# Kernel tuning notes

Hardware: AMD Instinct MI355X
Metric: run time of the kernel (lower is better)

Reference implementation:

```python
import jax, jax.numpy as jnp
import numpy as np

D_MODEL = 1024
NUM_EXPERTS = 8


def setup_inputs() -> dict:
    key = jax.random.key(0)
    k_x, k_wg, k_bg, k_we, k_be = jax.random.split(key, 5)
    B, S, D, E = 4, 2048, D_MODEL, NUM_EXPERTS
    x = jax.random.normal(k_x, (B, S, D), dtype=jnp.float32)
    # gate: nn.Linear(d_model, num_experts) -> weight [E, D], bias [E]
    Wg = jax.random.normal(k_wg, (E, D), dtype=jnp.float32) * 0.02
    bg = jax.random.normal(k_bg, (E,), dtype=jnp.float32) * 0.02
    # experts: E x nn.Linear(d_model, d_model) -> weights [E, D, D], biases [E, D]
    We = jax.random.normal(k_we, (E, D, D), dtype=jnp.float32) * 0.02
    be = jax.random.normal(k_be, (E, D), dtype=jnp.float32) * 0.02
    return {"x": x, "Wg": Wg, "bg": bg, "We": We, "be": be, "top_k": 2}


def reference(x, Wg, bg, We, be, top_k):
    # gate_scores: softmax over experts. x:[B,S,D], Wg:[E,D] -> [B,S,E]
    gate_scores = jax.nn.softmax(jnp.einsum("bsd,ed->bse", x, Wg) + bg, axis=-1)
    top_k_values, top_k_indices = jax.lax.top_k(gate_scores, top_k)  # [B,S,K]
    # dense all-expert compute (faithful to original): [B,S,D,E]
    expert_outputs = jnp.einsum("bsd,ekd->bske", x, We) + be.T  # be.T: [D,E]
    # gather top-k experts along last dim: idx broadcast over feature dim D
    top_k_outputs = jnp.take_along_axis(
        expert_outputs, top_k_indices[:, :, None, :], axis=-1
    )  # [B,S,D,K]
    weighted = (top_k_outputs * top_k_values[:, :, None, :]).sum(axis=-1)  # [B,S,D]
    return weighted
```

## Files before the change

### kernel.cpp

```cpp
#include <hip/hip_runtime.h>
#include <hip/hip_bf16.h>
#include <stdint.h>

#define D_MODEL 1024
#define NUM_EXPERTS 8
#define NBUCKET 16
#define BM 128
#define BN 128
#define BK 64
#define KSTEPS (D_MODEL / BK)
#define GATE_TOK 32
#define GATE_BLOCKS 256
#define CONV_BLOCKS 2048
#define NSEG (NUM_EXPERTS * KSTEPS * 1024 * 8)

typedef __bf16 bf16x8 __attribute__((ext_vector_type(8)));
typedef float f32x4 __attribute__((ext_vector_type(4)));
typedef unsigned short u16x8 __attribute__((ext_vector_type(8)));

__device__ __forceinline__ unsigned short f32_to_bf16_rne(float f) {
    union { float f; uint32_t u; } v;
    v.f = f;
    uint32_t u = v.u;
    u += 0x7FFFu + ((u >> 16) & 1u);
    return (unsigned short)(u >> 16);
}

__device__ __forceinline__ float bf16_to_f32(unsigned short h) {
    union { uint32_t u; float f; } v;
    v.u = ((uint32_t)h) << 16;
    return v.f;
}

__device__ __forceinline__ void gload_lds16(const unsigned short* g, unsigned short* l) {
    __builtin_amdgcn_global_load_lds(
        (const __attribute__((address_space(1))) void*)g,
        (__attribute__((address_space(3))) void*)l,
        16, 0, 0);
}

__global__ __launch_bounds__(512) void prep_kernel(
    const float* __restrict__ x, const float* __restrict__ Wg,
    const float* __restrict__ bg, const float* __restrict__ We, int T,
    int* __restrict__ counts, int* __restrict__ token_list,
    float* __restrict__ gate_list, unsigned short* __restrict__ xb,
    unsigned short* __restrict__ wbv)
{
    const int tid = threadIdx.x;

    if (blockIdx.x >= GATE_BLOCKS) {
        int g = (blockIdx.x - GATE_BLOCKS) * 512 + tid;
        int s   = g & 7;
        int kt  = (g >> 3) & (KSTEPS - 1);
        int n   = (g >> 7) & 1023;
        int e   = g >> 17;

        const float* sp = We + (size_t)g * 8;
        float4 a = ((const float4*)sp)[0];
        float4 b = ((const float4*)sp)[1];
        u16x8 o;
        o[0] = f32_to_bf16_rne(a.x);
        o[1] = f32_to_bf16_rne(a.y);
        o[2] = f32_to_bf16_rne(a.z);
        o[3] = f32_to_bf16_rne(a.w);
        o[4] = f32_to_bf16_rne(b.x);
        o[5] = f32_to_bf16_rne(b.y);
        o[6] = f32_to_bf16_rne(b.z);
        o[7] = f32_to_bf16_rne(b.w);

        int ss = s ^ (n & 7);
        unsigned short* dp =
            wbv + (((size_t)(e * KSTEPS + kt) * 1024 + n) * BK) + ss * 8;
        *(u16x8*)dp = o;
        return;
    }

    const int lane = tid & 63;
    const int wave = tid >> 6;
    const int tokBase = blockIdx.x * GATE_TOK;

    __shared__ float4 WgS[NUM_EXPERTS * 256];
    __shared__ double logitS[GATE_TOK][NUM_EXPERTS];
    __shared__ int cntS[NBUCKET];
    __shared__ int baseS[NBUCKET];

    if (tid < NBUCKET) cntS[tid] = 0;
#pragma unroll
    for (int i = 0; i < 4; i++)
        WgS[i * 512 + tid] = ((const float4*)Wg)[i * 512 + tid];
    __syncthreads();

    for (int tt = 0; tt < GATE_TOK / 8; tt++) {
        const int lt = wave * (GATE_TOK / 8) + tt;
        const int token = tokBase + lt;
        const float4* xr4 = (const float4*)(x + (size_t)token * D_MODEL);
        ushort4* xbr4 = (ushort4*)(xb + (size_t)token * D_MODEL);

        float4 xv[4];
#pragma unroll
        for (int q = 0; q < 4; q++) {
            float4 f = xr4[q * 64 + lane];
            xv[q] = f;
            ushort4 o;
            o.x = f32_to_bf16_rne(f.x);
            o.y = f32_to_bf16_rne(f.y);
            o.z = f32_to_bf16_rne(f.z);
            o.w = f32_to_bf16_rne(f.w);
            xbr4[q * 64 + lane] = o;
        }

        double acc[NUM_EXPERTS];
#pragma unroll
        for (int e = 0; e < NUM_EXPERTS; e++) {
            double a = 0.0;
#pragma unroll
            for (int q = 0; q < 4; q++) {
                float4 w = WgS[e * 256 + q * 64 + lane];
                a += (double)xv[q].x * (double)w.x;
                a += (double)xv[q].y * (double)w.y;
                a += (double)xv[q].z * (double)w.z;
                a += (double)xv[q].w * (double)w.w;
            }
            acc[e] = a;
        }
#pragma unroll
        for (int e = 0; e < NUM_EXPERTS; e++) {
            double a = acc[e];
            for (int off = 32; off > 0; off >>= 1) a += __shfl_xor(a, off, 64);
            acc[e] = a;
        }
        if (lane == 0) {
#pragma unroll
            for (int e = 0; e < NUM_EXPERTS; e++)
                logitS[lt][e] = acc[e] + (double)bg[e];
        }
    }
    __syncthreads();

    int i1 = 0, i2 = 0, o1 = 0, o2 = 0;
    double v1d = 0.0, v2d = 0.0;
    const int token2 = tokBase + tid;
    if (tid < GATE_TOK) {
        double lg[NUM_EXPERTS];
#pragma unroll
        for (int e = 0; e < NUM_EXPERTS; e++) lg[e] = logitS[tid][e];
        i1 = 0;
#pragma unroll
        for (int e = 1; e < NUM_EXPERTS; e++) if (lg[e] > lg[i1]) i1 = e;
        i2 = (i1 == 0) ? 1 : 0;
#pragma unroll
        for (int e = 0; e < NUM_EXPERTS; e++)
            if (e != i1 && lg[e] > lg[i2]) i2 = e;
        double m = lg[i1], den = 0.0;
#pragma unroll
        for (int e = 0; e < NUM_EXPERTS; e++) den += exp(lg[e] - m);
        v1d = exp(lg[i1] - m) / den;
        v2d = exp(lg[i2] - m) / den;
        o1 = atomicAdd(&cntS[i1], 1);
        o2 = atomicAdd(&cntS[8 + i2], 1);
    }
    __syncthreads();
    if (tid < NBUCKET) baseS[tid] = atomicAdd(&counts[tid], cntS[tid]);
    __syncthreads();
    if (tid < GATE_TOK) {
        int p1 = i1 * T + baseS[i1] + o1;
        token_list[p1] = token2;
        gate_list[p1]  = (float)v1d;
        int p2 = (8 + i2) * T + baseS[8 + i2] + o2;
        token_list[p2] = token2;
        gate_list[p2]  = (float)v2d;
    }
}

__global__ __launch_bounds__(512) void moe_gemm(
    const unsigned short* __restrict__ xb,
    const unsigned short* __restrict__ wb,
    const float* __restrict__ be,
    const int* __restrict__ counts,
    const int* __restrict__ token_list,
    const float* __restrict__ gate_list,
    unsigned short* __restrict__ ybuf,
    int T)
{
    const int bid = blockIdx.x;
    const int nt = bid & 7;
    const int rest = bid >> 3;
    const int vexp = rest & (NBUCKET - 1);
    const int mt = rest >> 4;
    const int e_w = vexp & 7;

    const int n_e = counts[vexp];
    const int m0 = mt * BM;
    if (m0 >= n_e) return;
    const int n0 = nt * BN;
    const int tid = threadIdx.x;

    __shared__ __align__(16) unsigned short As[2][BM * BK];
    __shared__ __align__(16) unsigned short Bs[2][BN * BK];
    __shared__ int   tokS[BM];
    __shared__ float gateS[BM];

    if (tid < BM) {
        int r = m0 + tid;
        int tk = 0; float gv = 0.f;
        if (r < n_e) {
            tk = token_list[vexp * T + r];
            gv = gate_list[vexp * T + r];
        }
        tokS[tid]  = tk;
        gateS[tid] = gv;
    }
    __syncthreads();

    const unsigned short* asrc[2];
#pragma unroll
    for (int i = 0; i < 2; i++) {
        int flat = i * 512 + tid;
        int r = flat >> 3, seg = flat & 7;
        int ss = seg ^ (r & 7);
        asrc[i] = xb + (size_t)tokS[r] * D_MODEL + ss * 8;
    }
    const unsigned short* bsrc =
        wb + (size_t)e_w * (KSTEPS * 1024 * BK) + (size_t)n0 * BK;

    const int wave = tid >> 6, lane = tid & 63;
    const int wm = (wave >> 2) * 64, wn = (wave & 3) * 32;
    const int frow = lane & 15;
    const int qq = lane >> 4;
    const int sw8 = frow & 7;

    f32x4 acc[4][2];
#pragma unroll
    for (int mi = 0; mi < 4; mi++)
#pragma unroll
        for (int ni = 0; ni < 2; ni++)
            acc[mi][ni] = (f32x4){0.f, 0.f, 0.f, 0.f};

#pragma unroll
    for (int i = 0; i < 2; i++) {
        int flat = i * 512 + tid;
        gload_lds16(asrc[i], &As[0][flat * 8]);
        gload_lds16(bsrc + flat * 8, &Bs[0][flat * 8]);
    }

#pragma unroll 2
    for (int kt = 0; kt < KSTEPS; kt++) {
        const int cur = kt & 1;
        if (kt + 1 < KSTEPS) {
#pragma unroll
            for (int i = 0; i < 2; i++) {
                int flat = i * 512 + tid;
                gload_lds16(asrc[i] + (kt + 1) * BK, &As[cur ^ 1][flat * 8]);
                gload_lds16(bsrc + (size_t)(kt + 1) * (1024 * BK) + flat * 8,
                            &Bs[cur ^ 1][flat * 8]);
            }
            asm volatile("s_waitcnt vmcnt(4)" ::: "memory");
        } else {
            asm volatile("s_waitcnt vmcnt(0)" ::: "memory");
        }
        __builtin_amdgcn_sched_barrier(0);
        __builtin_amdgcn_s_barrier();
        __builtin_amdgcn_sched_barrier(0);

#pragma unroll
        for (int ks = 0; ks < 2; ks++) {
            const int off = ((ks * 4 + qq) ^ sw8) * 8;
            bf16x8 af[4], bfv[2];
#pragma unroll
            for (int mi = 0; mi < 4; mi++)
                af[mi] = *(const bf16x8*)&As[cur][(wm + mi * 16 + frow) * BK + off];
#pragma unroll
            for (int ni = 0; ni < 2; ni++)
                bfv[ni] = *(const bf16x8*)&Bs[cur][(wn + ni * 16 + frow) * BK + off];
#pragma unroll
            for (int mi = 0; mi < 4; mi++)
#pragma unroll
                for (int ni = 0; ni < 2; ni++)
                    acc[mi][ni] = __builtin_amdgcn_mfma_f32_16x16x32_bf16(
                        af[mi], bfv[ni], acc[mi][ni], 0, 0, 0);
        }
        __builtin_amdgcn_sched_barrier(0);
        __builtin_amdgcn_s_barrier();
        __builtin_amdgcn_sched_barrier(0);
    }

    unsigned short* ybase = ybuf + (size_t)(vexp >> 3) * T * D_MODEL;
    const int rbase = (lane >> 4) * 4;
    const int col   = lane & 15;
#pragma unroll
    for (int mi = 0; mi < 4; mi++) {
#pragma unroll
        for (int r = 0; r < 4; r++) {
            int lrow = wm + mi * 16 + rbase + r;
            if (m0 + lrow < n_e) {
                int   tk = tokS[lrow];
                float gv = gateS[lrow];
                unsigned short* yr = ybase + (size_t)tk * D_MODEL;
#pragma unroll
                for (int ni = 0; ni < 2; ni++) {
                    int c = n0 + wn + ni * 16 + col;
                    float val = gv * (acc[mi][ni][r] + be[e_w * D_MODEL + c]);
                    yr[c] = f32_to_bf16_rne(val);
                }
            }
        }
    }
}

__global__ __launch_bounds__(256) void combine_kernel(
    const unsigned short* __restrict__ y0,
    const unsigned short* __restrict__ y1,
    float* __restrict__ out, int n4)
{
    int i = blockIdx.x * 256 + threadIdx.x;
    if (i >= n4) return;
    ushort4 a = ((const ushort4*)y0)[i];
    ushort4 b = ((const ushort4*)y1)[i];
    float4 o;
    o.x = bf16_to_f32(a.x) + bf16_to_f32(b.x);
    o.y = bf16_to_f32(a.y) + bf16_to_f32(b.y);
    o.z = bf16_to_f32(a.z) + bf16_to_f32(b.z);
    o.w = bf16_to_f32(a.w) + bf16_to_f32(b.w);
    ((float4*)out)[i] = o;
}

extern "C" void kernel_launch(void* const* d_in, const int* in_sizes, int n_in,
                              void* d_out, int out_size, void* d_ws, size_t ws_size,
                              hipStream_t stream) {
    const float* x  = (const float*)d_in[0];
    const float* Wg = (const float*)d_in[1];
    const float* bg = (const float*)d_in[2];
    const float* We = (const float*)d_in[3];
    const float* be = (const float*)d_in[4];

    const int T = in_sizes[0] / D_MODEL;

    char* ws = (char*)d_ws;
    unsigned short* xb = (unsigned short*)ws;
    size_t off = (size_t)T * D_MODEL * 2;
    unsigned short* wbv = (unsigned short*)(ws + off);
    off += (size_t)NUM_EXPERTS * D_MODEL * D_MODEL * 2;
    int* counts = (int*)(ws + off);         off += 256;
    int* token_list = (int*)(ws + off);     off += (size_t)NBUCKET * T * 4;
    float* gate_list = (float*)(ws + off);  off += (size_t)NBUCKET * T * 4;
    unsigned short* ybuf = (unsigned short*)(ws + off);
    off += (size_t)2 * T * D_MODEL * 2;

    hipMemsetAsync(counts, 0, 256, stream);

    prep_kernel<<<GATE_BLOCKS + CONV_BLOCKS, 512, 0, stream>>>(
        x, Wg, bg, We, T, counts, token_list, gate_list, xb, wbv);

    const int MT = (T + BM - 1) / BM;
    moe_gemm<<<MT * NBUCKET * 8, 512, 0, stream>>>(
        xb, wbv, be, counts, token_list, gate_list, ybuf, T);

    int n4c = T * D_MODEL / 4;
    combine_kernel<<<(n4c + 255) / 256, 256, 0, stream>>>(
        ybuf, ybuf + (size_t)T * D_MODEL, (float*)d_out, n4c);
}
```

Before: 231.6 us.

## Split prep kernel into separate convert and finer-grained gate kernels

Splits the fused prep kernel into a standalone weight-conversion kernel and a gate kernel. The gate kernel now uses 256-thread blocks with 8 tokens each, giving 1024 gate blocks instead of 256, so gating is spread over more CUs. Each wave handles two tokens, reading Wg directly from global memory once per pair, and the cross-lane reduction goes through shared memory plus three shuffles instead of six-step shuffles per expert. The cost is an extra kernel launch, and the gate and conversion work now run one after the other instead of sharing a single grid.

```diff
diff --git a/kernel.cpp b/kernel.cpp
--- a/kernel.cpp
+++ b/kernel.cpp
@@ -9,9 +9,7 @@
 #define BN 128
 #define BK 64
 #define KSTEPS (D_MODEL / BK)
-#define GATE_TOK 32
-#define GATE_BLOCKS 256
-#define CONV_BLOCKS 2048
+#define GATE_TOK 8
 #define NSEG (NUM_EXPERTS * KSTEPS * 1024 * 8)
 
 typedef __bf16 bf16x8 __attribute__((ext_vector_type(8)));
@@ -39,68 +37,36 @@
         16, 0, 0);
 }
 
-__global__ __launch_bounds__(512) void prep_kernel(
+__global__ __launch_bounds__(256) void gate_kernel(
     const float* __restrict__ x, const float* __restrict__ Wg,
-    const float* __restrict__ bg, const float* __restrict__ We, int T,
+    const float* __restrict__ bg, int T,
     int* __restrict__ counts, int* __restrict__ token_list,
-    float* __restrict__ gate_list, unsigned short* __restrict__ xb,
-    unsigned short* __restrict__ wbv)
+    float* __restrict__ gate_list, unsigned short* __restrict__ xb)
 {
-    const int tid = threadIdx.x;
-
-    if (blockIdx.x >= GATE_BLOCKS) {
-        int g = (blockIdx.x - GATE_BLOCKS) * 512 + tid;
-        int s   = g & 7;
-        int kt  = (g >> 3) & (KSTEPS - 1);
-        int n   = (g >> 7) & 1023;
-        int e   = g >> 17;
-
-        const float* sp = We + (size_t)g * 8;
-        float4 a = ((const float4*)sp)[0];
-        float4 b = ((const float4*)sp)[1];
-        u16x8 o;
-        o[0] = f32_to_bf16_rne(a.x);
-        o[1] = f32_to_bf16_rne(a.y);
-        o[2] = f32_to_bf16_rne(a.z);
-        o[3] = f32_to_bf16_rne(a.w);
-        o[4] = f32_to_bf16_rne(b.x);
-        o[5] = f32_to_bf16_rne(b.y);
-        o[6] = f32_to_bf16_rne(b.z);
-        o[7] = f32_to_bf16_rne(b.w);
-
-        int ss = s ^ (n & 7);
-        unsigned short* dp =
-            wbv + (((size_t)(e * KSTEPS + kt) * 1024 + n) * BK) + ss * 8;
-        *(u16x8*)dp = o;
-        return;
-    }
-
+    const int tid  = threadIdx.x;
     const int lane = tid & 63;
     const int wave = tid >> 6;
     const int tokBase = blockIdx.x * GATE_TOK;
 
-    __shared__ float4 WgS[NUM_EXPERTS * 256];
+    __shared__ double red[4][NUM_EXPERTS][65];
     __shared__ double logitS[GATE_TOK][NUM_EXPERTS];
     __shared__ int cntS[NBUCKET];
     __shared__ int baseS[NBUCKET];
 
     if (tid < NBUCKET) cntS[tid] = 0;
-#pragma unroll
-    for (int i = 0; i < 4; i++)
-        WgS[i * 512 + tid] = ((const float4*)Wg)[i * 512 + tid];
-    __syncthreads();
-
-    for (int tt = 0; tt < GATE_TOK / 8; tt++) {
-        const int lt = wave * (GATE_TOK / 8) + tt;
-        const int token = tokBase + lt;
+
+    const float4* Wg4 = (const float4*)Wg;
+
+    float4 xv[2][4];
+#pragma unroll
+    for (int t = 0; t < 2; t++) {
+        const int token = tokBase + wave * 2 + t;
         const float4* xr4 = (const float4*)(x + (size_t)token * D_MODEL);
         ushort4* xbr4 = (ushort4*)(xb + (size_t)token * D_MODEL);
-
-        float4 xv[4];
 #pragma unroll
         for (int q = 0; q < 4; q++) {
             float4 f = xr4[q * 64 + lane];
-            xv[q] = f;
+            xv[t][q] = f;
             ushort4 o;
             o.x = f32_to_bf16_rne(f.x);
             o.y = f32_to_bf16_rne(f.y);
@@ -108,32 +74,43 @@
             o.w = f32_to_bf16_rne(f.w);
             xbr4[q * 64 + lane] = o;
         }
-
-        double acc[NUM_EXPERTS];
-#pragma unroll
-        for (int e = 0; e < NUM_EXPERTS; e++) {
-            double a = 0.0;
-#pragma unroll
-            for (int q = 0; q < 4; q++) {
-                float4 w = WgS[e * 256 + q * 64 + lane];
-                a += (double)xv[q].x * (double)w.x;
-                a += (double)xv[q].y * (double)w.y;
-                a += (double)xv[q].z * (double)w.z;
-                a += (double)xv[q].w * (double)w.w;
+    }
+
+    double acc[2][NUM_EXPERTS];
+#pragma unroll
+    for (int t = 0; t < 2; t++)
+#pragma unroll
+        for (int e = 0; e < NUM_EXPERTS; e++) acc[t][e] = 0.0;
+#pragma unroll
+    for (int e = 0; e < NUM_EXPERTS; e++) {
+#pragma unroll
+        for (int q = 0; q < 4; q++) {
+            float4 w = Wg4[e * 256 + q * 64 + lane];
+#pragma unroll
+            for (int t = 0; t < 2; t++) {
+                acc[t][e] += (double)xv[t][q].x * (double)w.x;
+                acc[t][e] += (double)xv[t][q].y * (double)w.y;
+                acc[t][e] += (double)xv[t][q].z * (double)w.z;
+                acc[t][e] += (double)xv[t][q].w * (double)w.w;
             }
-            acc[e] = a;
-        }
-#pragma unroll
-        for (int e = 0; e < NUM_EXPERTS; e++) {
-            double a = acc[e];
-            for (int off = 32; off > 0; off >>= 1) a += __shfl_xor(a, off, 64);
-            acc[e] = a;
-        }
-        if (lane == 0) {
-#pragma unroll
-            for (int e = 0; e < NUM_EXPERTS; e++)
-                logitS[lt][e] = acc[e] + (double)bg[e];
-        }
+        }
+    }
+
+    const int e2 = lane >> 3, g = lane & 7;
+#pragma unroll
+    for (int t = 0; t < 2; t++) {
+#pragma unroll
+        for (int e = 0; e < NUM_EXPERTS; e++)
+            red[wave][e][lane] = acc[t][e];
+        double s = 0.0;
+#pragma unroll
+        for (int j = 0; j < 8; j++)
+            s += red[wave][e2][g * 8 + j];
+        s += __shfl_xor(s, 1, 64);
+        s += __shfl_xor(s, 2, 64);
+        s += __shfl_xor(s, 4, 64);
+        if (g == 0)
+            logitS[wave * 2 + t][e2] = s + (double)bg[e2];
     }
     __syncthreads();
 
@@ -170,6 +147,34 @@
         token_list[p2] = token2;
         gate_list[p2]  = (float)v2d;
     }
+}
+
+__global__ __launch_bounds__(256) void convert_kernel(
+    const float* __restrict__ src, unsigned short* __restrict__ dst)
+{
+    int g = blockIdx.x * 256 + threadIdx.x;
+    int s   = g & 7;
+    int kt  = (g >> 3) & (KSTEPS - 1);
+    int n   = (g >> 7) & 1023;
+    int e   = g >> 17;
+
+    const float* sp = src + (size_t)g * 8;
+    float4 a = ((const float4*)sp)[0];
+    float4 b = ((const float4*)sp)[1];
+    u16x8 o;
+    o[0] = f32_to_bf16_rne(a.x);
+    o[1] = f32_to_bf16_rne(a.y);
+    o[2] = f32_to_bf16_rne(a.z);
+    o[3] = f32_to_bf16_rne(a.w);
+    o[4] = f32_to_bf16_rne(b.x);
+    o[5] = f32_to_bf16_rne(b.y);
+    o[6] = f32_to_bf16_rne(b.z);
+    o[7] = f32_to_bf16_rne(b.w);
+
+    int ss = s ^ (n & 7);
+    unsigned short* dp =
+        dst + (((size_t)(e * KSTEPS + kt) * 1024 + n) * BK) + ss * 8;
+    *(u16x8*)dp = o;
 }
 
 __global__ __launch_bounds__(512) void moe_gemm(
@@ -348,8 +353,10 @@
 
     hipMemsetAsync(counts, 0, 256, stream);
 
-    prep_kernel<<<GATE_BLOCKS + CONV_BLOCKS, 512, 0, stream>>>(
-        x, Wg, bg, We, T, counts, token_list, gate_list, xb, wbv);
+    convert_kernel<<<NSEG / 256, 256, 0, stream>>>(We, wbv);
+
+    gate_kernel<<<T / GATE_TOK, 256, 0, stream>>>(
+        x, Wg, bg, T, counts, token_list, gate_list, xb);
 
     const int MT = (T + BM - 1) / BM;
     moe_gemm<<<MT * NBUCKET * 8, 512, 0, stream>>>(
```

Measured after the change: 200.2 us. 13.6% less time.
